# Kernel optimization log

Hardware: AMD Instinct MI355X
Metric: run time of the kernel (lower is better)

The kernel has to match this reference:

```python
import jax, jax.numpy as jnp
import numpy as np

N_NODES = 50000
N_EDGES = 800000
F_IN = 64
HID = 64
N_CLASSES = 10
N_GRAPHS = 64


def setup_inputs() -> dict:
    key = jax.random.key(0)
    ks = jax.random.split(key, 16)
    x = jax.random.normal(ks[0], (N_NODES, F_IN), dtype=jnp.float32)
    edge_index = jax.random.randint(ks[1], (2, N_EDGES), 0, N_NODES, dtype=jnp.int32)
    supernode_mask = jax.random.bernoulli(ks[2], 0.1, (N_NODES,))
    edge_mask = jax.random.bernoulli(ks[3], 0.5, (N_EDGES,)).astype(jnp.float32)
    batch = jnp.sort(jax.random.randint(ks[4], (N_NODES,), 0, N_GRAPHS, dtype=jnp.int32))
    def glorot(k, fan_in, fan_out):
        s = jnp.sqrt(6.0 / (fan_in + fan_out))
        return jax.random.uniform(k, (fan_in, fan_out), jnp.float32, -s, s)
    W1 = glorot(ks[5], F_IN, HID); b1 = jnp.zeros((HID,), jnp.float32)
    W2 = glorot(ks[6], HID, HID); b2 = jnp.zeros((HID,), jnp.float32)
    W3 = glorot(ks[7], HID, HID); b3 = jnp.zeros((HID,), jnp.float32)
    Wl = glorot(ks[8], HID, N_CLASSES); bl = jnp.zeros((N_CLASSES,), jnp.float32)
    return {"x": x, "edge_index": edge_index, "supernode_mask": supernode_mask,
            "edge_mask": edge_mask, "batch": batch,
            "W1": W1, "b1": b1, "W2": W2, "b2": b2, "W3": W3, "b3": b3,
            "Wl": Wl, "bl": bl}


def reference(x, edge_index, supernode_mask, edge_mask, batch,
              W1, b1, W2, b2, W3, b3, Wl, bl):
    N = x.shape[0]
    src, dst = edge_index[0], edge_index[1]

    # SimpleConv('add'): weighted sum of source features into targets
    x2 = jax.ops.segment_sum(x[src] * edge_mask[:, None], dst, num_segments=N)
    x = jnp.where(supernode_mask[:, None], x2, x)

    # GCN normalization with self-loops: deg = 1 + in-degree, norm = d^-1/2[src]*d^-1/2[dst]
    deg = jax.ops.segment_sum(jnp.ones((src.shape[0],), x.dtype), dst, num_segments=N) + 1.0
    dinv = jax.lax.rsqrt(deg)
    coef = dinv[src] * dinv[dst]          # [E]
    self_coef = (dinv * dinv)[:, None]    # self-loop contribution [N,1]

    def gcn(h, W, b):
        h = h @ W  # small GEMM [N, HID]
        agg = jax.ops.segment_sum(h[src] * coef[:, None], dst, num_segments=N)
        return agg + h * self_coef + b

    h = jax.nn.relu(gcn(x, W1, b1))
    h = jax.nn.relu(gcn(h, W2, b2))
    h = gcn(h, W3, b3)

    # global_mean_pool over graphs
    sums = jax.ops.segment_sum(h, batch, num_segments=N_GRAPHS)
    cnt = jax.ops.segment_sum(jnp.ones((N,), h.dtype), batch, num_segments=N_GRAPHS)
    pooled = sums / jnp.maximum(cnt, 1.0)[:, None]

    # dropout is identity in eval mode
    return pooled @ Wl + bl
```

## Files before the change

kernel.cpp:

```cpp
#include <hip/hip_runtime.h>

#define FEAT 64
#define NGRAPH 64
#define POOL_CHUNKS 8
#define CAP 96
#define SUB 24
#define FILL_CHUNKS 256
#define FILLB (FILL_CHUNKS * 8)

typedef short bf16x8 __attribute__((ext_vector_type(8)));
typedef float f32x4 __attribute__((ext_vector_type(4)));
union FragU { uint4 u4; bf16x8 h; };


__device__ __forceinline__ unsigned int pack_bf16(float a, float b) {
    unsigned int ua = __float_as_uint(a), ub = __float_as_uint(b);
    ua = (ua + 0x7FFFu + ((ua >> 16) & 1u)) >> 16;
    ub = (ub + 0x7FFFu + ((ub >> 16) & 1u)) >> 16;
    return ua | (ub << 16);
}
__device__ __forceinline__ float bf_lo(unsigned int w) {
    return __uint_as_float(w << 16);
}
__device__ __forceinline__ float bf_hi(unsigned int w) {
    return __uint_as_float(w & 0xFFFF0000u);
}
__device__ __forceinline__ bool read_mask(const void* sm, int i, int fl) {
    if (fl & 2) return ((const float*)sm)[i] != 0.f;
    if (fl & 1) return ((const unsigned char*)sm)[i] != 0;
    return ((const int*)sm)[i] != 0;
}
__device__ __forceinline__ int lbound(const int* a, int n, int key) {
    int lo = 0, hi = n;
    while (lo < hi) {
        int mid = (lo + hi) >> 1;
        if (a[mid] < key) lo = mid + 1; else hi = mid;
    }
    return lo;
}

__global__ __launch_bounds__(256) void k_fillprep(const int* __restrict__ ei,
                                                  const float* __restrict__ emask,
                                                  unsigned int* __restrict__ cnt,
                                                  unsigned int* __restrict__ csr,
                                                  int E, int ce,
                                                  const float* __restrict__ x,
                                                  unsigned int* __restrict__ u, int n8,
                                                  const float* __restrict__ W1,
                                                  const float* __restrict__ W2,
                                                  const float* __restrict__ W3,
                                                  unsigned int* __restrict__ wt,
                                                  const unsigned int* __restrict__ m,
                                                  int nwords, int* __restrict__ flag) {
    int bid = blockIdx.x;
    if (bid < FILLB) {
        int p = bid & 7;
        int e0 = (bid >> 3) * ce;
        int e1 = min(e0 + ce, E);
        for (int e = e0 + (int)threadIdx.x * 4; e + 3 < e1; e += 256 * 4) {
            const int4 d4 = *(const int4*)(ei + E + e);
            const int4 s4 = *(const int4*)(ei + e);
            const float4 m4 = *(const float4*)(emask + e);
#pragma unroll
            for (int k = 0; k < 4; ++k) {
                int dst = (k == 0) ? d4.x : (k == 1) ? d4.y : (k == 2) ? d4.z : d4.w;
                if ((dst >> 13) != p) continue;
                int src = (k == 0) ? s4.x : (k == 1) ? s4.y : (k == 2) ? s4.z : s4.w;
                float mw = (k == 0) ? m4.x : (k == 1) ? m4.y : (k == 2) ? m4.z : m4.w;
                unsigned int slot = atomicAdd(&cnt[dst * 4 + k], 1u);
                if (slot < SUB) {
                    unsigned int word = (unsigned int)src;
                    if (mw != 0.f) word |= 0x10000u;
                    csr[(size_t)dst * CAP + k * SUB + slot] = word;
                }
            }
        }
        return;
    }
    int t = (bid - FILLB) * 256 + threadIdx.x;
    if (t < n8) {
        const float4 a = *(const float4*)(x + (size_t)t * 8);
        const float4 b = *(const float4*)(x + (size_t)t * 8 + 4);
        uint4 p;
        p.x = pack_bf16(a.x, a.y);
        p.y = pack_bf16(a.z, a.w);
        p.z = pack_bf16(b.x, b.y);
        p.w = pack_bf16(b.z, b.w);
        *(uint4*)(u + (size_t)t * 4) = p;
    }
    if (t < 3 * 2048) {
        int mm = t >> 11, w = t & 2047;
        int c = w >> 5, kw = w & 31;
        const float* W = (mm == 0) ? W1 : ((mm == 1) ? W2 : W3);
        wt[t] = pack_bf16(W[(2 * kw) * 64 + c], W[(2 * kw + 1) * 64 + c]);
    }
    if (t < nwords) {
        unsigned int w = m[t];
        if (w == 0x3F800000u) atomicOr(flag, 2);
        else if (w > 1u) atomicOr(flag, 1);
    }
}

__device__ __forceinline__ int vmap(int vj, int p1, int p2, int p3) {
    return (vj < p1) ? vj
         : (vj < p2) ? SUB + (vj - p1)
         : (vj < p3) ? 2 * SUB + (vj - p2)
         : 3 * SUB + (vj - p3);
}

__global__ __launch_bounds__(256) void k_sup(const float* __restrict__ x,
                                             const uint4* __restrict__ cnt4,
                                             const unsigned int* __restrict__ csr,
                                             const void* __restrict__ sm,
                                             const int* __restrict__ flag,
                                             unsigned int* __restrict__ u, int N) {
    int t = blockIdx.x * 256 + threadIdx.x;
    int i = t >> 6, lane = t & 63;
    if (i >= N) return;
    int fl = *flag;
    if (!read_mask(sm, i, fl)) return;
    int g = lane >> 4, q = lane & 15;
    uint4 c4 = cnt4[i];
    int l0 = min((int)c4.x, SUB), l1 = min((int)c4.y, SUB);
    int l2 = min((int)c4.z, SUB), l3 = min((int)c4.w, SUB);
    int p1 = l0, p2 = l0 + l1, p3 = p2 + l2;
    int tot = p3 + l3;
    const unsigned int* row = csr + (size_t)i * CAP;
    float4 acc = {0.f, 0.f, 0.f, 0.f};
    for (int j0 = 0; j0 < tot; j0 += 64) {
        int c = min(64, tot - j0);
        unsigned int w_l = (lane < c) ? row[vmap(j0 + lane, p1, p2, p3)] : 0u;
        int rounds4 = (c + 3) & ~3;
#pragma unroll 2
        for (int j = 0; j < rounds4; j += 4) {
            unsigned int wd = __shfl(w_l, j + g);
            if (wd & 0x10000u) {
                int s = (int)(wd & 0xFFFFu);
                const float4 v = *(const float4*)(x + (size_t)s * FEAT + q * 4);
                acc.x += v.x; acc.y += v.y; acc.z += v.z; acc.w += v.w;
            }
        }
    }
#pragma unroll
    for (int m = 16; m < 64; m <<= 1) {
        acc.x += __shfl_xor(acc.x, m);
        acc.y += __shfl_xor(acc.y, m);
        acc.z += __shfl_xor(acc.z, m);
        acc.w += __shfl_xor(acc.w, m);
    }
    if (g == 0) {
        uint2 p;
        p.x = pack_bf16(acc.x, acc.y);
        p.y = pack_bf16(acc.z, acc.w);
        *(uint2*)(u + (size_t)i * 32 + q * 2) = p;
    }
}

__global__ __launch_bounds__(256) void k_gemm_mfma(const unsigned int* __restrict__ u_in,
                                                   const unsigned int* __restrict__ wbfT,
                                                   const uint4* __restrict__ cnt4,
                                                   unsigned int* __restrict__ hd, int N) {
    int wid = threadIdx.x >> 6, lane = threadIdx.x & 63;
    int row0 = (blockIdx.x * 4 + wid) * 16;
    if (row0 >= N) return;
    int r = lane & 15, half = lane >> 4;
    f32x4 acc0 = {0.f, 0.f, 0.f, 0.f}, acc1 = acc0, acc2 = acc0, acc3 = acc0;
#pragma unroll
    for (int ks = 0; ks < 2; ++ks) {
        FragU a;
        a.u4 = *(const uint4*)(u_in + (size_t)(row0 + r) * 32 + ks * 16 + half * 4);
        FragU b0, b1, b2, b3;
        b0.u4 = *(const uint4*)(wbfT + (0 * 16 + r) * 32 + ks * 16 + half * 4);
        b1.u4 = *(const uint4*)(wbfT + (1 * 16 + r) * 32 + ks * 16 + half * 4);
        b2.u4 = *(const uint4*)(wbfT + (2 * 16 + r) * 32 + ks * 16 + half * 4);
        b3.u4 = *(const uint4*)(wbfT + (3 * 16 + r) * 32 + ks * 16 + half * 4);
        acc0 = __builtin_amdgcn_mfma_f32_16x16x32_bf16(a.h, b0.h, acc0, 0, 0, 0);
        acc1 = __builtin_amdgcn_mfma_f32_16x16x32_bf16(a.h, b1.h, acc1, 0, 0, 0);
        acc2 = __builtin_amdgcn_mfma_f32_16x16x32_bf16(a.h, b2.h, acc2, 0, 0, 0);
        acc3 = __builtin_amdgcn_mfma_f32_16x16x32_bf16(a.h, b3.h, acc3, 0, 0, 0);
    }
    uint4 c0 = cnt4[row0 + half * 4 + 0], c1 = cnt4[row0 + half * 4 + 1];
    uint4 c2 = cnt4[row0 + half * 4 + 2], c3 = cnt4[row0 + half * 4 + 3];
    float dd0 = rsqrtf((float)(c0.x + c0.y + c0.z + c0.w) + 1.f);
    float dd1 = rsqrtf((float)(c1.x + c1.y + c1.z + c1.w) + 1.f);
    float dd2 = rsqrtf((float)(c2.x + c2.y + c2.z + c2.w) + 1.f);
    float dd3 = rsqrtf((float)(c3.x + c3.y + c3.z + c3.w) + 1.f);
#pragma unroll
    for (int t = 0; t < 4; ++t) {
        const f32x4 acc = (t == 0) ? acc0 : (t == 1) ? acc1 : (t == 2) ? acc2 : acc3;
        float v0 = acc[0] * dd0, v1 = acc[1] * dd1, v2 = acc[2] * dd2, v3 = acc[3] * dd3;
        float o0 = __shfl_xor(v0, 1), o1 = __shfl_xor(v1, 1),
              o2 = __shfl_xor(v2, 1), o3 = __shfl_xor(v3, 1);
        if ((r & 1) == 0) {
            size_t base = (size_t)(row0 + half * 4) * 32 + t * 8 + (r >> 1);
            hd[base + 0 * 32] = pack_bf16(v0, o0);
            hd[base + 1 * 32] = pack_bf16(v1, o1);
            hd[base + 2 * 32] = pack_bf16(v2, o2);
            hd[base + 3 * 32] = pack_bf16(v3, o3);
        }
    }
}

__global__ __launch_bounds__(256) void k_gather(const unsigned int* __restrict__ hd,
                                                const float* __restrict__ b,
                                                const uint4* __restrict__ cnt4,
                                                const unsigned int* __restrict__ csr,
                                                unsigned int* __restrict__ u_out,
                                                int N, int do_relu) {
    int t = blockIdx.x * 256 + threadIdx.x;
    int i = t >> 6, lane = t & 63;
    if (i >= N) return;
    int g = lane >> 3, q = lane & 7;
    uint4 c4 = cnt4[i];
    int deg = (int)(c4.x + c4.y + c4.z + c4.w);
    int l0 = min((int)c4.x, SUB), l1 = min((int)c4.y, SUB);
    int l2 = min((int)c4.z, SUB), l3 = min((int)c4.w, SUB);
    int p1 = l0, p2 = l0 + l1, p3 = p2 + l2;
    int tot = p3 + l3;
    const unsigned int* row = csr + (size_t)i * CAP;
    float acc[8] = {0.f, 0.f, 0.f, 0.f, 0.f, 0.f, 0.f, 0.f};
    for (int j0 = 0; j0 < tot; j0 += 64) {
        int c = min(64, tot - j0);
        int s_l = (lane < c) ? (int)(row[vmap(j0 + lane, p1, p2, p3)] & 0xFFFFu) : 0;
        int rounds8 = (c + 7) & ~7;
#pragma unroll 2
        for (int j = 0; j < rounds8; j += 8) {
            int jj = j + g;
            int s = __shfl(s_l, jj);
            if (jj < c) {
                const uint4 v = *(const uint4*)(hd + (size_t)s * 32 + q * 4);
                acc[0] += bf_lo(v.x); acc[1] += bf_hi(v.x);
                acc[2] += bf_lo(v.y); acc[3] += bf_hi(v.y);
                acc[4] += bf_lo(v.z); acc[5] += bf_hi(v.z);
                acc[6] += bf_lo(v.w); acc[7] += bf_hi(v.w);
            }
        }
    }
#pragma unroll
    for (int m = 8; m < 64; m <<= 1) {
#pragma unroll
        for (int k = 0; k < 8; ++k) acc[k] += __shfl_xor(acc[k], m);
    }
    if (g == 0) {
        float dd = rsqrtf((float)deg + 1.f);
        const uint4 hv = *(const uint4*)(hd + (size_t)i * 32 + q * 4);
        const float4 b0 = *(const float4*)(b + q * 8);
        const float4 b1 = *(const float4*)(b + q * 8 + 4);
        float r[8];
        r[0] = (acc[0] + bf_lo(hv.x)) * dd + b0.x;
        r[1] = (acc[1] + bf_hi(hv.x)) * dd + b0.y;
        r[2] = (acc[2] + bf_lo(hv.y)) * dd + b0.z;
        r[3] = (acc[3] + bf_hi(hv.y)) * dd + b0.w;
        r[4] = (acc[4] + bf_lo(hv.z)) * dd + b1.x;
        r[5] = (acc[5] + bf_hi(hv.z)) * dd + b1.y;
        r[6] = (acc[6] + bf_lo(hv.w)) * dd + b1.z;
        r[7] = (acc[7] + bf_hi(hv.w)) * dd + b1.w;
        if (do_relu) {
#pragma unroll
            for (int k = 0; k < 8; ++k) r[k] = fmaxf(r[k], 0.f);
        }
        uint4 p;
        p.x = pack_bf16(r[0], r[1]);
        p.y = pack_bf16(r[2], r[3]);
        p.z = pack_bf16(r[4], r[5]);
        p.w = pack_bf16(r[6], r[7]);
        *(uint4*)(u_out + (size_t)i * 32 + q * 4) = p;
    }
}

__global__ __launch_bounds__(256) void k_pool(const unsigned int* __restrict__ xb,
                                              const int* __restrict__ batch,
                                              float* __restrict__ pooled, int N) {
    int g = blockIdx.x >> 3, c = blockIdx.x & (POOL_CHUNKS - 1);
    int lo = lbound(batch, N, g);
    int hi = lbound(batch, N, g + 1);
    int len = hi - lo;
    int t = threadIdx.x, lane = t & 63, sub = t >> 6;
    int a = lo + (int)(((long long)len * c) / POOL_CHUNKS);
    int bnd = lo + (int)(((long long)len * (c + 1)) / POOL_CHUNKS);
    float s = 0.f;
    int w = lane >> 1;
    bool hi_half = lane & 1;
    for (int i = a + sub; i < bnd; i += 4) {
        unsigned int word = xb[(size_t)i * 32 + w];
        s += hi_half ? bf_hi(word) : bf_lo(word);
    }
    __shared__ float red[4][64];
    red[sub][lane] = s;
    __syncthreads();
    if (sub == 0) {
        float tot = red[0][lane] + red[1][lane] + red[2][lane] + red[3][lane];
        unsafeAtomicAdd(&pooled[g * FEAT + lane], tot);
    }
}

__global__ __launch_bounds__(640) void k_logits(const float* __restrict__ pooled,
                                                const int* __restrict__ batch, int N,
                                                const float* __restrict__ Wl,
                                                const float* __restrict__ bl,
                                                float* __restrict__ out) {
    __shared__ float inv[NGRAPH];
    int t = threadIdx.x;
    if (t < NGRAPH) {
        int lo = lbound(batch, N, t);
        int hi = lbound(batch, N, t + 1);
        inv[t] = 1.f / fmaxf((float)(hi - lo), 1.f);
    }
    __syncthreads();
    if (t >= NGRAPH * 10) return;
    int g = t / 10, cls = t % 10;
    float s = 0.f;
#pragma unroll
    for (int f = 0; f < 64; ++f) s += pooled[g * 64 + f] * Wl[f * 10 + cls];
    out[t] = s * inv[g] + bl[cls];
}

extern "C" void kernel_launch(void* const* d_in, const int* in_sizes, int n_in,
                              void* d_out, int out_size, void* d_ws, size_t ws_size,
                              hipStream_t stream) {
    const float* x = (const float*)d_in[0];
    const int* ei = (const int*)d_in[1];
    const void* sm = d_in[2];
    const float* emask = (const float*)d_in[3];
    const int* batch = (const int*)d_in[4];
    const float* W1 = (const float*)d_in[5];
    const float* b1 = (const float*)d_in[6];
    const float* W2 = (const float*)d_in[7];
    const float* b2 = (const float*)d_in[8];
    const float* W3 = (const float*)d_in[9];
    const float* b3 = (const float*)d_in[10];
    const float* Wl = (const float*)d_in[11];
    const float* bl = (const float*)d_in[12];

    const int N = in_sizes[0] / FEAT;
    const int E = in_sizes[1] / 2;

    float* wsf = (float*)d_ws;
    size_t off = 0;
    unsigned int* ua = (unsigned int*)(wsf + off); off += (size_t)N * 32;
    unsigned int* ub = (unsigned int*)(wsf + off); off += (size_t)N * 32;
    unsigned int* hd = (unsigned int*)(wsf + off); off += (size_t)N * 32;
    unsigned int* wbf = (unsigned int*)(wsf + off); off += 3 * 2048;
    unsigned int* csr = (unsigned int*)(wsf + off); off += (size_t)N * CAP;
    unsigned int* cnt = (unsigned int*)(wsf + off); off += (size_t)N * 4;
    float* pooled = wsf + off;         off += NGRAPH * FEAT;
    int* flag = (int*)(wsf + off);     off += 1;

    const int wblocks = (N * 64 + 255) / 256;
    const int gemm_blocks = (N / 16 + 3) / 4;
    const int prep_blocks = (N * 8 + 255) / 256;
    const int ce = ((E + FILL_CHUNKS - 1) / FILL_CHUNKS + 3) & ~3;

    hipMemsetAsync(cnt, 0, (size_t)(N * 4 + NGRAPH * FEAT + 1) * 4, stream);
    k_fillprep<<<FILLB + prep_blocks, 256, 0, stream>>>(
        ei, emask, cnt, csr, E, ce,
        x, ua, N * 8, W1, W2, W3, wbf, (const unsigned int*)sm, N / 4, flag);
    k_sup<<<wblocks, 256, 0, stream>>>(x, (const uint4*)cnt, csr, sm, flag, ua, N);

    k_gemm_mfma<<<gemm_blocks, 256, 0, stream>>>(ua, wbf + 0 * 2048, (const uint4*)cnt, hd, N);
    k_gather<<<wblocks, 256, 0, stream>>>(hd, b1, (const uint4*)cnt, csr, ub, N, 1);
    k_gemm_mfma<<<gemm_blocks, 256, 0, stream>>>(ub, wbf + 1 * 2048, (const uint4*)cnt, hd, N);
    k_gather<<<wblocks, 256, 0, stream>>>(hd, b2, (const uint4*)cnt, csr, ua, N, 1);
    k_gemm_mfma<<<gemm_blocks, 256, 0, stream>>>(ua, wbf + 2 * 2048, (const uint4*)cnt, hd, N);
    k_gather<<<wblocks, 256, 0, stream>>>(hd, b3, (const uint4*)cnt, csr, ub, N, 0);

    k_pool<<<NGRAPH * POOL_CHUNKS, 256, 0, stream>>>(ub, batch, pooled, N);
    k_logits<<<1, 640, 0, stream>>>(pooled, batch, N, Wl, bl, (float*)d_out);
}
```

Baseline: 201.3 us.

## Fuse post-fill pipeline into one persistent cooperative kernel with grid syncs

Replaces the chain of nine kernel launches (supernode aggregation, three GEMM+gather layers, pooling, logits) with a single cooperative persistent kernel. Waves loop over rows and tiles with grid-stride scheduling, and each stage is separated by grid.sync(). This targets launch gaps and tail effects between many short kernels. In exchange it adds the cost of the grid-wide barriers, and the fixed grid size may lower occupancy or memory parallelism in the gather phases. The old multi-kernel path is kept as a fallback if the cooperative launch fails.

```diff
diff --git a/kernel.cpp b/kernel.cpp
--- a/kernel.cpp
+++ b/kernel.cpp
@@ -1,4 +1,7 @@
 #include <hip/hip_runtime.h>
+#include <hip/hip_cooperative_groups.h>
+
+namespace cg = cooperative_groups;
 
 #define FEAT 64
 #define NGRAPH 64
@@ -7,6 +10,7 @@
 #define SUB 24
 #define FILL_CHUNKS 256
 #define FILLB (FILL_CHUNKS * 8)
+#define NCU 256
 
 typedef short bf16x8 __attribute__((ext_vector_type(8)));
 typedef float f32x4 __attribute__((ext_vector_type(4)));
@@ -37,6 +41,12 @@
         if (a[mid] < key) lo = mid + 1; else hi = mid;
     }
     return lo;
+}
+__device__ __forceinline__ int vmap(int vj, int p1, int p2, int p3) {
+    return (vj < p1) ? vj
+         : (vj < p2) ? SUB + (vj - p1)
+         : (vj < p3) ? 2 * SUB + (vj - p2)
+         : 3 * SUB + (vj - p3);
 }
 
 __global__ __launch_bounds__(256) void k_fillprep(const int* __restrict__ ei,
@@ -101,12 +111,166 @@
     }
 }
 
-__device__ __forceinline__ int vmap(int vj, int p1, int p2, int p3) {
-    return (vj < p1) ? vj
-         : (vj < p2) ? SUB + (vj - p1)
-         : (vj < p3) ? 2 * SUB + (vj - p2)
-         : 3 * SUB + (vj - p3);
-}
+
+__device__ __forceinline__ void sup_phase(const float* __restrict__ x,
+                                          const uint4* __restrict__ cnt4,
+                                          const unsigned int* __restrict__ csr,
+                                          const void* __restrict__ sm, int fl,
+                                          unsigned int* __restrict__ u,
+                                          int N, int gwave, int nwave, int lane) {
+    int g = lane >> 4, q = lane & 15;
+    for (int i = gwave; i < N; i += nwave) {
+        if (!read_mask(sm, i, fl)) continue;
+        uint4 c4 = cnt4[i];
+        int l0 = min((int)c4.x, SUB), l1 = min((int)c4.y, SUB);
+        int l2 = min((int)c4.z, SUB), l3 = min((int)c4.w, SUB);
+        int p1 = l0, p2 = l0 + l1, p3 = p2 + l2;
+        int tot = p3 + l3;
+        const unsigned int* row = csr + (size_t)i * CAP;
+        float4 acc = {0.f, 0.f, 0.f, 0.f};
+        for (int j0 = 0; j0 < tot; j0 += 64) {
+            int c = min(64, tot - j0);
+            unsigned int w_l = (lane < c) ? row[vmap(j0 + lane, p1, p2, p3)] : 0u;
+            int rounds4 = (c + 3) & ~3;
+#pragma unroll 2
+            for (int j = 0; j < rounds4; j += 4) {
+                unsigned int wd = __shfl(w_l, j + g);
+                if (wd & 0x10000u) {
+                    int s = (int)(wd & 0xFFFFu);
+                    const float4 v = *(const float4*)(x + (size_t)s * FEAT + q * 4);
+                    acc.x += v.x; acc.y += v.y; acc.z += v.z; acc.w += v.w;
+                }
+            }
+        }
+#pragma unroll
+        for (int m = 16; m < 64; m <<= 1) {
+            acc.x += __shfl_xor(acc.x, m);
+            acc.y += __shfl_xor(acc.y, m);
+            acc.z += __shfl_xor(acc.z, m);
+            acc.w += __shfl_xor(acc.w, m);
+        }
+        if (g == 0) {
+            uint2 p;
+            p.x = pack_bf16(acc.x, acc.y);
+            p.y = pack_bf16(acc.z, acc.w);
+            *(uint2*)(u + (size_t)i * 32 + q * 2) = p;
+        }
+    }
+}
+
+__device__ __forceinline__ void gemm_phase(const unsigned int* __restrict__ u_in,
+                                           const unsigned int* __restrict__ wbfT,
+                                           const uint4* __restrict__ cnt4,
+                                           unsigned int* __restrict__ hd,
+                                           int ntiles, int gwave, int nwave, int lane) {
+    int r = lane & 15, half = lane >> 4;
+    for (int tile = gwave; tile < ntiles; tile += nwave) {
+        int row0 = tile * 16;
+        f32x4 acc0 = {0.f, 0.f, 0.f, 0.f}, acc1 = acc0, acc2 = acc0, acc3 = acc0;
+#pragma unroll
+        for (int ks = 0; ks < 2; ++ks) {
+            FragU a;
+            a.u4 = *(const uint4*)(u_in + (size_t)(row0 + r) * 32 + ks * 16 + half * 4);
+            FragU b0, b1, b2, b3;
+            b0.u4 = *(const uint4*)(wbfT + (0 * 16 + r) * 32 + ks * 16 + half * 4);
+            b1.u4 = *(const uint4*)(wbfT + (1 * 16 + r) * 32 + ks * 16 + half * 4);
+            b2.u4 = *(const uint4*)(wbfT + (2 * 16 + r) * 32 + ks * 16 + half * 4);
+            b3.u4 = *(const uint4*)(wbfT + (3 * 16 + r) * 32 + ks * 16 + half * 4);
+            acc0 = __builtin_amdgcn_mfma_f32_16x16x32_bf16(a.h, b0.h, acc0, 0, 0, 0);
+            acc1 = __builtin_amdgcn_mfma_f32_16x16x32_bf16(a.h, b1.h, acc1, 0, 0, 0);
+            acc2 = __builtin_amdgcn_mfma_f32_16x16x32_bf16(a.h, b2.h, acc2, 0, 0, 0);
+            acc3 = __builtin_amdgcn_mfma_f32_16x16x32_bf16(a.h, b3.h, acc3, 0, 0, 0);
+        }
+        uint4 c0 = cnt4[row0 + half * 4 + 0], c1 = cnt4[row0 + half * 4 + 1];
+        uint4 c2 = cnt4[row0 + half * 4 + 2], c3 = cnt4[row0 + half * 4 + 3];
+        float dd0 = rsqrtf((float)(c0.x + c0.y + c0.z + c0.w) + 1.f);
+        float dd1 = rsqrtf((float)(c1.x + c1.y + c1.z + c1.w) + 1.f);
+        float dd2 = rsqrtf((float)(c2.x + c2.y + c2.z + c2.w) + 1.f);
+        float dd3 = rsqrtf((float)(c3.x + c3.y + c3.z + c3.w) + 1.f);
+#pragma unroll
+        for (int t = 0; t < 4; ++t) {
+            const f32x4 acc = (t == 0) ? acc0 : (t == 1) ? acc1 : (t == 2) ? acc2 : acc3;
+            float v0 = acc[0] * dd0, v1 = acc[1] * dd1, v2 = acc[2] * dd2, v3 = acc[3] * dd3;
+            float o0 = __shfl_xor(v0, 1), o1 = __shfl_xor(v1, 1),
+                  o2 = __shfl_xor(v2, 1), o3 = __shfl_xor(v3, 1);
+            if ((r & 1) == 0) {
+                size_t base = (size_t)(row0 + half * 4) * 32 + t * 8 + (r >> 1);
+                hd[base + 0 * 32] = pack_bf16(v0, o0);
+                hd[base + 1 * 32] = pack_bf16(v1, o1);
+                hd[base + 2 * 32] = pack_bf16(v2, o2);
+                hd[base + 3 * 32] = pack_bf16(v3, o3);
+            }
+        }
+    }
+}
+
+__device__ __forceinline__ void gather_phase(const unsigned int* __restrict__ hd,
+                                             const float* __restrict__ b,
+                                             const uint4* __restrict__ cnt4,
+                                             const unsigned int* __restrict__ csr,
+                                             unsigned int* __restrict__ u_out,
+                                             int N, int do_relu,
+                                             int gwave, int nwave, int lane) {
+    int g = lane >> 3, q = lane & 7;
+    for (int i = gwave; i < N; i += nwave) {
+        uint4 c4 = cnt4[i];
+        int deg = (int)(c4.x + c4.y + c4.z + c4.w);
+        int l0 = min((int)c4.x, SUB), l1 = min((int)c4.y, SUB);
+        int l2 = min((int)c4.z, SUB), l3 = min((int)c4.w, SUB);
+        int p1 = l0, p2 = l0 + l1, p3 = p2 + l2;
+        int tot = p3 + l3;
+        const unsigned int* row = csr + (size_t)i * CAP;
+        float acc[8] = {0.f, 0.f, 0.f, 0.f, 0.f, 0.f, 0.f, 0.f};
+        for (int j0 = 0; j0 < tot; j0 += 64) {
+            int c = min(64, tot - j0);
+            int s_l = (lane < c) ? (int)(row[vmap(j0 + lane, p1, p2, p3)] & 0xFFFFu) : 0;
+            int rounds8 = (c + 7) & ~7;
+#pragma unroll 2
+            for (int j = 0; j < rounds8; j += 8) {
+                int jj = j + g;
+                int s = __shfl(s_l, jj);
+                if (jj < c) {
+                    const uint4 v = *(const uint4*)(hd + (size_t)s * 32 + q * 4);
+                    acc[0] += bf_lo(v.x); acc[1] += bf_hi(v.x);
+                    acc[2] += bf_lo(v.y); acc[3] += bf_hi(v.y);
+                    acc[4] += bf_lo(v.z); acc[5] += bf_hi(v.z);
+                    acc[6] += bf_lo(v.w); acc[7] += bf_hi(v.w);
+                }
+            }
+        }
+#pragma unroll
+        for (int m = 8; m < 64; m <<= 1) {
+#pragma unroll
+            for (int k = 0; k < 8; ++k) acc[k] += __shfl_xor(acc[k], m);
+        }
+        if (g == 0) {
+            float dd = rsqrtf((float)deg + 1.f);
+            const uint4 hv = *(const uint4*)(hd + (size_t)i * 32 + q * 4);
+            const float4 b0 = *(const float4*)(b + q * 8);
+            const float4 b1 = *(const float4*)(b + q * 8 + 4);
+            float r[8];
+            r[0] = (acc[0] + bf_lo(hv.x)) * dd + b0.x;
+            r[1] = (acc[1] + bf_hi(hv.x)) * dd + b0.y;
+            r[2] = (acc[2] + bf_lo(hv.y)) * dd + b0.z;
+            r[3] = (acc[3] + bf_hi(hv.y)) * dd + b0.w;
+            r[4] = (acc[4] + bf_lo(hv.z)) * dd + b1.x;
+            r[5] = (acc[5] + bf_hi(hv.z)) * dd + b1.y;
+            r[6] = (acc[6] + bf_lo(hv.w)) * dd + b1.z;
+            r[7] = (acc[7] + bf_hi(hv.w)) * dd + b1.w;
+            if (do_relu) {
+#pragma unroll
+                for (int k = 0; k < 8; ++k) r[k] = fmaxf(r[k], 0.f);
+            }
+            uint4 p;
+            p.x = pack_bf16(r[0], r[1]);
+            p.y = pack_bf16(r[2], r[3]);
+            p.z = pack_bf16(r[4], r[5]);
+            p.w = pack_bf16(r[6], r[7]);
+            *(uint4*)(u_out + (size_t)i * 32 + q * 4) = p;
+        }
+    }
+}
+
 
 __global__ __launch_bounds__(256) void k_sup(const float* __restrict__ x,
                                              const uint4* __restrict__ cnt4,
@@ -114,91 +278,19 @@
                                              const void* __restrict__ sm,
                                              const int* __restrict__ flag,
                                              unsigned int* __restrict__ u, int N) {
-    int t = blockIdx.x * 256 + threadIdx.x;
-    int i = t >> 6, lane = t & 63;
-    if (i >= N) return;
-    int fl = *flag;
-    if (!read_mask(sm, i, fl)) return;
-    int g = lane >> 4, q = lane & 15;
-    uint4 c4 = cnt4[i];
-    int l0 = min((int)c4.x, SUB), l1 = min((int)c4.y, SUB);
-    int l2 = min((int)c4.z, SUB), l3 = min((int)c4.w, SUB);
-    int p1 = l0, p2 = l0 + l1, p3 = p2 + l2;
-    int tot = p3 + l3;
-    const unsigned int* row = csr + (size_t)i * CAP;
-    float4 acc = {0.f, 0.f, 0.f, 0.f};
-    for (int j0 = 0; j0 < tot; j0 += 64) {
-        int c = min(64, tot - j0);
-        unsigned int w_l = (lane < c) ? row[vmap(j0 + lane, p1, p2, p3)] : 0u;
-        int rounds4 = (c + 3) & ~3;
-#pragma unroll 2
-        for (int j = 0; j < rounds4; j += 4) {
-            unsigned int wd = __shfl(w_l, j + g);
-            if (wd & 0x10000u) {
-                int s = (int)(wd & 0xFFFFu);
-                const float4 v = *(const float4*)(x + (size_t)s * FEAT + q * 4);
-                acc.x += v.x; acc.y += v.y; acc.z += v.z; acc.w += v.w;
-            }
-        }
-    }
-#pragma unroll
-    for (int m = 16; m < 64; m <<= 1) {
-        acc.x += __shfl_xor(acc.x, m);
-        acc.y += __shfl_xor(acc.y, m);
-        acc.z += __shfl_xor(acc.z, m);
-        acc.w += __shfl_xor(acc.w, m);
-    }
-    if (g == 0) {
-        uint2 p;
-        p.x = pack_bf16(acc.x, acc.y);
-        p.y = pack_bf16(acc.z, acc.w);
-        *(uint2*)(u + (size_t)i * 32 + q * 2) = p;
-    }
+    int wid = threadIdx.x >> 6, lane = threadIdx.x & 63;
+    sup_phase(x, cnt4, csr, sm, *flag, u, N,
+              blockIdx.x * 4 + wid, gridDim.x * 4, lane);
 }
 
 __global__ __launch_bounds__(256) void k_gemm_mfma(const unsigned int* __restrict__ u_in,
                                                    const unsigned int* __restrict__ wbfT,
                                                    const uint4* __restrict__ cnt4,
-                                                   unsigned int* __restrict__ hd, int N) {
+                                                   unsigned int* __restrict__ hd,
+                                                   int ntiles) {
     int wid = threadIdx.x >> 6, lane = threadIdx.x & 63;
-    int row0 = (blockIdx.x * 4 + wid) * 16;
-    if (row0 >= N) return;
-    int r = lane & 15, half = lane >> 4;
-    f32x4 acc0 = {0.f, 0.f, 0.f, 0.f}, acc1 = acc0, acc2 = acc0, acc3 = acc0;
-#pragma unroll
-    for (int ks = 0; ks < 2; ++ks) {
-        FragU a;
-        a.u4 = *(const uint4*)(u_in + (size_t)(row0 + r) * 32 + ks * 16 + half * 4);
-        FragU b0, b1, b2, b3;
-        b0.u4 = *(const uint4*)(wbfT + (0 * 16 + r) * 32 + ks * 16 + half * 4);
-        b1.u4 = *(const uint4*)(wbfT + (1 * 16 + r) * 32 + ks * 16 + half * 4);
-        b2.u4 = *(const uint4*)(wbfT + (2 * 16 + r) * 32 + ks * 16 + half * 4);
-        b3.u4 = *(const uint4*)(wbfT + (3 * 16 + r) * 32 + ks * 16 + half * 4);
-        acc0 = __builtin_amdgcn_mfma_f32_16x16x32_bf16(a.h, b0.h, acc0, 0, 0, 0);
-        acc1 = __builtin_amdgcn_mfma_f32_16x16x32_bf16(a.h, b1.h, acc1, 0, 0, 0);
-        acc2 = __builtin_amdgcn_mfma_f32_16x16x32_bf16(a.h, b2.h, acc2, 0, 0, 0);
-        acc3 = __builtin_amdgcn_mfma_f32_16x16x32_bf16(a.h, b3.h, acc3, 0, 0, 0);
-    }
-    uint4 c0 = cnt4[row0 + half * 4 + 0], c1 = cnt4[row0 + half * 4 + 1];
-    uint4 c2 = cnt4[row0 + half * 4 + 2], c3 = cnt4[row0 + half * 4 + 3];
-    float dd0 = rsqrtf((float)(c0.x + c0.y + c0.z + c0.w) + 1.f);
-    float dd1 = rsqrtf((float)(c1.x + c1.y + c1.z + c1.w) + 1.f);
-    float dd2 = rsqrtf((float)(c2.x + c2.y + c2.z + c2.w) + 1.f);
-    float dd3 = rsqrtf((float)(c3.x + c3.y + c3.z + c3.w) + 1.f);
-#pragma unroll
-    for (int t = 0; t < 4; ++t) {
-        const f32x4 acc = (t == 0) ? acc0 : (t == 1) ? acc1 : (t == 2) ? acc2 : acc3;
-        float v0 = acc[0] * dd0, v1 = acc[1] * dd1, v2 = acc[2] * dd2, v3 = acc[3] * dd3;
-        float o0 = __shfl_xor(v0, 1), o1 = __shfl_xor(v1, 1),
-              o2 = __shfl_xor(v2, 1), o3 = __shfl_xor(v3, 1);
-        if ((r & 1) == 0) {
-            size_t base = (size_t)(row0 + half * 4) * 32 + t * 8 + (r >> 1);
-            hd[base + 0 * 32] = pack_bf16(v0, o0);
-            hd[base + 1 * 32] = pack_bf16(v1, o1);
-            hd[base + 2 * 32] = pack_bf16(v2, o2);
-            hd[base + 3 * 32] = pack_bf16(v3, o3);
-        }
-    }
+    gemm_phase(u_in, wbfT, cnt4, hd, ntiles,
+               blockIdx.x * 4 + wid, gridDim.x * 4, lane);
 }
 
 __global__ __launch_bounds__(256) void k_gather(const unsigned int* __restrict__ hd,
@@ -207,65 +299,9 @@
                                                 const unsigned int* __restrict__ csr,
                                                 unsigned int* __restrict__ u_out,
                                                 int N, int do_relu) {
-    int t = blockIdx.x * 256 + threadIdx.x;
-    int i = t >> 6, lane = t & 63;
-    if (i >= N) return;
-    int g = lane >> 3, q = lane & 7;
-    uint4 c4 = cnt4[i];
-    int deg = (int)(c4.x + c4.y + c4.z + c4.w);
-    int l0 = min((int)c4.x, SUB), l1 = min((int)c4.y, SUB);
-    int l2 = min((int)c4.z, SUB), l3 = min((int)c4.w, SUB);
-    int p1 = l0, p2 = l0 + l1, p3 = p2 + l2;
-    int tot = p3 + l3;
-    const unsigned int* row = csr + (size_t)i * CAP;
-    float acc[8] = {0.f, 0.f, 0.f, 0.f, 0.f, 0.f, 0.f, 0.f};
-    for (int j0 = 0; j0 < tot; j0 += 64) {
-        int c = min(64, tot - j0);
-        int s_l = (lane < c) ? (int)(row[vmap(j0 + lane, p1, p2, p3)] & 0xFFFFu) : 0;
-        int rounds8 = (c + 7) & ~7;
-#pragma unroll 2
-        for (int j = 0; j < rounds8; j += 8) {
-            int jj = j + g;
-            int s = __shfl(s_l, jj);
-            if (jj < c) {
-                const uint4 v = *(const uint4*)(hd + (size_t)s * 32 + q * 4);
-                acc[0] += bf_lo(v.x); acc[1] += bf_hi(v.x);
-                acc[2] += bf_lo(v.y); acc[3] += bf_hi(v.y);
-                acc[4] += bf_lo(v.z); acc[5] += bf_hi(v.z);
-                acc[6] += bf_lo(v.w); acc[7] += bf_hi(v.w);
-            }
-        }
-    }
-#pragma unroll
-    for (int m = 8; m < 64; m <<= 1) {
-#pragma unroll
-        for (int k = 0; k < 8; ++k) acc[k] += __shfl_xor(acc[k], m);
-    }
-    if (g == 0) {
-        float dd = rsqrtf((float)deg + 1.f);
-        const uint4 hv = *(const uint4*)(hd + (size_t)i * 32 + q * 4);
-        const float4 b0 = *(const float4*)(b + q * 8);
-        const float4 b1 = *(const float4*)(b + q * 8 + 4);
-        float r[8];
-        r[0] = (acc[0] + bf_lo(hv.x)) * dd + b0.x;
-        r[1] = (acc[1] + bf_hi(hv.x)) * dd + b0.y;
-        r[2] = (acc[2] + bf_lo(hv.y)) * dd + b0.z;
-        r[3] = (acc[3] + bf_hi(hv.y)) * dd + b0.w;
-        r[4] = (acc[4] + bf_lo(hv.z)) * dd + b1.x;
-        r[5] = (acc[5] + bf_hi(hv.z)) * dd + b1.y;
-        r[6] = (acc[6] + bf_lo(hv.w)) * dd + b1.z;
-        r[7] = (acc[7] + bf_hi(hv.w)) * dd + b1.w;
-        if (do_relu) {
-#pragma unroll
-            for (int k = 0; k < 8; ++k) r[k] = fmaxf(r[k], 0.f);
-        }
-        uint4 p;
-        p.x = pack_bf16(r[0], r[1]);
-        p.y = pack_bf16(r[2], r[3]);
-        p.z = pack_bf16(r[4], r[5]);
-        p.w = pack_bf16(r[6], r[7]);
-        *(uint4*)(u_out + (size_t)i * 32 + q * 4) = p;
-    }
+    int wid = threadIdx.x >> 6, lane = threadIdx.x & 63;
+    gather_phase(hd, b, cnt4, csr, u_out, N, do_relu,
+                 blockIdx.x * 4 + wid, gridDim.x * 4, lane);
 }
 
 __global__ __launch_bounds__(256) void k_pool(const unsigned int* __restrict__ xb,
@@ -315,6 +351,85 @@
     out[t] = s * inv[g] + bl[cls];
 }
 
+
+__global__ __launch_bounds__(256, 4) void k_main(const float* __restrict__ x,
+                                                 const void* __restrict__ sm,
+                                                 const int* __restrict__ flag,
+                                                 const uint4* __restrict__ cnt4,
+                                                 const unsigned int* __restrict__ csr,
+                                                 unsigned int* __restrict__ ua,
+                                                 unsigned int* __restrict__ ub,
+                                                 unsigned int* __restrict__ hd,
+                                                 const unsigned int* __restrict__ wbf,
+                                                 const float* __restrict__ b1,
+                                                 const float* __restrict__ b2,
+                                                 const float* __restrict__ b3,
+                                                 const int* __restrict__ batch,
+                                                 const float* __restrict__ Wl,
+                                                 const float* __restrict__ bl,
+                                                 float* __restrict__ pooled,
+                                                 float* __restrict__ out, int N) {
+    cg::grid_group grid = cg::this_grid();
+    __shared__ float red[4][64];
+    int wid = threadIdx.x >> 6, lane = threadIdx.x & 63;
+    int gwave = blockIdx.x * 4 + wid;
+    int nwave = gridDim.x * 4;
+    int ntiles = N / 16;
+    int fl = *flag;
+
+    sup_phase(x, cnt4, csr, sm, fl, ua, N, gwave, nwave, lane);
+    grid.sync();
+    gemm_phase(ua, wbf + 0 * 2048, cnt4, hd, ntiles, gwave, nwave, lane);
+    grid.sync();
+    gather_phase(hd, b1, cnt4, csr, ub, N, 1, gwave, nwave, lane);
+    grid.sync();
+    gemm_phase(ub, wbf + 1 * 2048, cnt4, hd, ntiles, gwave, nwave, lane);
+    grid.sync();
+    gather_phase(hd, b2, cnt4, csr, ua, N, 1, gwave, nwave, lane);
+    grid.sync();
+    gemm_phase(ua, wbf + 2 * 2048, cnt4, hd, ntiles, gwave, nwave, lane);
+    grid.sync();
+    gather_phase(hd, b3, cnt4, csr, ub, N, 0, gwave, nwave, lane);
+    grid.sync();
+
+    for (int pb = blockIdx.x; pb < NGRAPH * POOL_CHUNKS; pb += gridDim.x) {
+        int g = pb >> 3, c = pb & (POOL_CHUNKS - 1);
+        int lo = lbound(batch, N, g);
+        int hi = lbound(batch, N, g + 1);
+        int len = hi - lo;
+        int a = lo + (int)(((long long)len * c) / POOL_CHUNKS);
+        int bnd = lo + (int)(((long long)len * (c + 1)) / POOL_CHUNKS);
+        float s = 0.f;
+        int w = lane >> 1;
+        bool hi_half = lane & 1;
+        for (int i = a + wid; i < bnd; i += 4) {
+            unsigned int word = ub[(size_t)i * 32 + w];
+            s += hi_half ? bf_hi(word) : bf_lo(word);
+        }
+        red[wid][lane] = s;
+        __syncthreads();
+        if (wid == 0) {
+            float tot = red[0][lane] + red[1][lane] + red[2][lane] + red[3][lane];
+            unsafeAtomicAdd(&pooled[g * FEAT + lane], tot);
+        }
+        __syncthreads();
+    }
+    grid.sync();
+
+    if (blockIdx.x == 0) {
+        for (int t = threadIdx.x; t < NGRAPH * 10; t += 256) {
+            int g = t / 10, cls = t % 10;
+            int lo = lbound(batch, N, g);
+            int hi = lbound(batch, N, g + 1);
+            float inv = 1.f / fmaxf((float)(hi - lo), 1.f);
+            float s = 0.f;
+#pragma unroll
+            for (int f = 0; f < 64; ++f) s += pooled[g * 64 + f] * Wl[f * 10 + cls];
+            out[t] = s * inv + bl[cls];
+        }
+    }
+}
+
 extern "C" void kernel_launch(void* const* d_in, const int* in_sizes, int n_in,
                               void* d_out, int out_size, void* d_ws, size_t ws_size,
                               hipStream_t stream) {
@@ -355,15 +470,40 @@
     k_fillprep<<<FILLB + prep_blocks, 256, 0, stream>>>(
         ei, emask, cnt, csr, E, ce,
         x, ua, N * 8, W1, W2, W3, wbf, (const unsigned int*)sm, N / 4, flag);
-    k_sup<<<wblocks, 256, 0, stream>>>(x, (const uint4*)cnt, csr, sm, flag, ua, N);
-
-    k_gemm_mfma<<<gemm_blocks, 256, 0, stream>>>(ua, wbf + 0 * 2048, (const uint4*)cnt, hd, N);
-    k_gather<<<wblocks, 256, 0, stream>>>(hd, b1, (const uint4*)cnt, csr, ub, N, 1);
-    k_gemm_mfma<<<gemm_blocks, 256, 0, stream>>>(ub, wbf + 1 * 2048, (const uint4*)cnt, hd, N);
-    k_gather<<<wblocks, 256, 0, stream>>>(hd, b2, (const uint4*)cnt, csr, ua, N, 1);
-    k_gemm_mfma<<<gemm_blocks, 256, 0, stream>>>(ua, wbf + 2 * 2048, (const uint4*)cnt, hd, N);
-    k_gather<<<wblocks, 256, 0, stream>>>(hd, b3, (const uint4*)cnt, csr, ub, N, 0);
-
-    k_pool<<<NGRAPH * POOL_CHUNKS, 256, 0, stream>>>(ub, batch, pooled, N);
-    k_logits<<<1, 640, 0, stream>>>(pooled, batch, N, Wl, bl, (float*)d_out);
-}
+
+    const uint4* cnt4 = (const uint4*)cnt;
+    float* outp = (float*)d_out;
+    int Nv = N;
+
+    int maxb = 0;
+    hipError_t oerr = hipOccupancyMaxActiveBlocksPerMultiprocessor(
+        &maxb, (const void*)k_main, 256, 0);
+    int coop_blocks = (oerr == hipSuccess) ? maxb * NCU : 0;
+    if (coop_blocks > 2048) coop_blocks = 2048;
+
+    bool coop_ok = false;
+    if (coop_blocks >= 512) {
+        void* args[] = {(void*)&x, (void*)&sm, (void*)&flag, (void*)&cnt4,
+                        (void*)&csr, (void*)&ua, (void*)&ub, (void*)&hd,
+                        (void*)&wbf, (void*)&b1, (void*)&b2, (void*)&b3,
+                        (void*)&batch, (void*)&Wl, (void*)&bl, (void*)&pooled,
+                        (void*)&outp, (void*)&Nv};
+        hipError_t lerr = hipLaunchCooperativeKernel((const void*)k_main,
+                                                     dim3(coop_blocks), dim3(256),
+                                                     args, 0, stream);
+        coop_ok = (lerr == hipSuccess);
+        if (!coop_ok) (void)hipGetLastError();
+    }
+
+    if (!coop_ok) {
+        k_sup<<<wblocks, 256, 0, stream>>>(x, cnt4, csr, sm, flag, ua, N);
+        k_gemm_mfma<<<gemm_blocks, 256, 0, stream>>>(ua, wbf + 0 * 2048, cnt4, hd, N / 16);
+        k_gather<<<wblocks, 256, 0, stream>>>(hd, b1, cnt4, csr, ub, N, 1);
+        k_gemm_mfma<<<gemm_blocks, 256, 0, stream>>>(ub, wbf + 1 * 2048, cnt4, hd, N / 16);
+        k_gather<<<wblocks, 256, 0, stream>>>(hd, b2, cnt4, csr, ua, N, 1);
+        k_gemm_mfma<<<gemm_blocks, 256, 0, stream>>>(ua, wbf + 2 * 2048, cnt4, hd, N / 16);
+        k_gather<<<wblocks, 256, 0, stream>>>(hd, b3, cnt4, csr, ub, N, 0);
+        k_pool<<<NGRAPH * POOL_CHUNKS, 256, 0, stream>>>(ub, batch, pooled, N);
+        k_logits<<<1, 640, 0, stream>>>(pooled, batch, N, Wl, bl, outp);
+    }
+}
```

New measurement: 791.2 us. +293.1%, slower.
